# Optimization experiments

Measured on AMD Instinct MI355X. Metric: run time of the kernel, lower is better.

## Reference

```python
import jax, jax.numpy as jnp
import numpy as np

T, IN, M, C, OUT = 8192, 1024, 64, 16, 1024  # time, input, trace, context, output


def _ln(x, eps=1e-5):
    mu = jnp.mean(x, axis=-1, keepdims=True)
    var = jnp.var(x, axis=-1, keepdims=True)
    return (x - mu) * jax.lax.rsqrt(var + eps)


def _mish(x):
    return x * jnp.tanh(jax.nn.softplus(x))


def setup_inputs() -> dict:
    key = jax.random.key(0)
    ks = jax.random.split(key, 8)

    def w(k, o, i):
        return (jax.random.normal(k, (o, i), jnp.float32) / np.sqrt(i).astype(np.float32))

    return {
        "x": jax.random.normal(ks[0], (T, IN), jnp.float32),
        "state0": jnp.zeros((1, M, C), jnp.float32),  # real part of complex zero init
        "start": jax.random.uniform(ks[1], (T,)) < 0.002,  # sparse episode resets
        "next_done": jnp.zeros((T,), bool),  # unused by the sequential-equivalent math
        "a": jnp.linspace(1e-6, 0.5, M, dtype=jnp.float32),  # ffa.init decay
        "bf": (2.0 * jnp.pi / jnp.linspace(1.0, 1024.0, C)).astype(jnp.float32),  # ffa.init freqs
        "pre_w": w(ks[2], M, IN), "pre_b": jnp.zeros((M,), jnp.float32),
        "skip_w": w(ks[3], OUT, IN), "skip_b": jnp.zeros((OUT,), jnp.float32),
        "mix_w1": w(ks[4], M * C, 2 * M * C), "mix_b1": jnp.zeros((M * C,), jnp.float32),
        "mix_w2": w(ks[5], M * C, M * C), "mix_b2": jnp.zeros((M * C,), jnp.float32),
        "mix_w3": w(ks[6], OUT, M * C), "mix_b3": jnp.zeros((OUT,), jnp.float32),
    }


def _forward(x, state0, start, a, bf, pre_w, pre_b, skip_w, skip_b,
             mix_w1, mix_b1, mix_w2, mix_b2, mix_w3, mix_b3):
    Tn = x.shape[0]
    # pre = softplus(Linear(LayerNorm(x)))  -> [T, M]
    pre = jax.nn.softplus(_ln(x) @ pre_w.T + pre_b)
    # one-step FFA decay gamma[m,c] = exp(-|a_m| + i*b_c)
    la = jnp.broadcast_to(-jnp.abs(a)[:, None], (a.shape[0], bf.shape[0]))
    lb = jnp.broadcast_to(bf[None, :], la.shape)
    gamma = jnp.exp(jax.lax.complex(la, lb))  # [M, C] complex64
    # reset monoid: s_t = A_t * s_{t-1} + b_t,  A_t = 0 where episode starts
    A = jnp.where(start[:, None, None], jnp.zeros((), gamma.dtype), gamma[None])  # [T,M,C]
    b_el = jnp.broadcast_to(pre[:, :, None].astype(gamma.dtype), A.shape)  # [T,M,C]
    s_init = state0.astype(gamma.dtype)  # [1, M, C]
    b_el = b_el.at[0].add(A[0] * s_init[0])  # fold carried state into first element

    def combine(lhs, rhs):
        Al, bl = lhs
        Ar, br = rhs
        return Ar * Al, Ar * bl + br

    _, s = jax.lax.associative_scan(combine, (A, b_el))  # s: [T, M, C] states at every t

    s_flat = s.reshape(Tn, M * C)
    # global (all-element) complex mean / real std normalization, as in the source
    scaled = (s_flat - jnp.mean(s_flat)) / (1e-6 + jnp.std(s_flat))
    z = jnp.concatenate([scaled.real, scaled.imag], axis=-1)  # [T, 2*M*C]
    z = _mish(z @ mix_w1.T + mix_b1)
    z = _mish(z @ mix_w2.T + mix_b2)
    z = z @ mix_w3.T + mix_b3  # [T, OUT]
    out = _ln(z + (x @ skip_w.T + skip_b))
    return out, s[-1:]


def reference(x, state0, start, next_done, a, bf, pre_w, pre_b, skip_w, skip_b,
              mix_w1, mix_b1, mix_w2, mix_b2, mix_w3, mix_b3):
    return _forward(x, state0, start, a, bf, pre_w, pre_b, skip_w, skip_b,
                    mix_w1, mix_b1, mix_w2, mix_b2, mix_w3, mix_b3)
```

## Files before the change

### kernel.cpp

```cpp
#include <hip/hip_runtime.h>
#include <hip/hip_bf16.h>

#define T_    8192
#define INDIM 1024
#define MTR   64
#define CCTX  16
#define MC    1024
#define NOUT  1024
#define CHUNK 64
#define NCH   128

using bf16x8 = __attribute__((ext_vector_type(8))) short;
using f32x4  = __attribute__((ext_vector_type(4))) float;

__device__ __forceinline__ unsigned short f2bf(float f) {
  unsigned int u = __builtin_bit_cast(unsigned int, f);
  u += 0x7fffu + ((u >> 16) & 1u);
  return (unsigned short)(u >> 16);
}
__device__ __forceinline__ float bf2f(unsigned short u) {
  return __builtin_bit_cast(float, (unsigned int)u << 16);
}

__device__ __forceinline__ float mish_f(float v) {
  float u = __expf(v);
  float w = u * (u + 2.f);
  return (v > 20.f) ? v : v * __fdividef(w, w + 2.f);
}

typedef __attribute__((address_space(1))) void gas_void;
typedef __attribute__((address_space(3))) void las_void;

__device__ __forceinline__ void gload_lds16(const void* g, void* l) {
  __builtin_amdgcn_global_load_lds((gas_void*)g, (las_void*)l, 16, 0, 0);
}

__device__ __forceinline__ float2 block_sum2(float s, float ss, float* sbuf) {
#pragma unroll
  for (int off = 32; off > 0; off >>= 1) {
    s  += __shfl_down(s, off);
    ss += __shfl_down(ss, off);
  }
  if ((threadIdx.x & 63) == 0) {
    sbuf[(threadIdx.x >> 6) * 2]     = s;
    sbuf[(threadIdx.x >> 6) * 2 + 1] = ss;
  }
  __syncthreads();
  return make_float2(sbuf[0] + sbuf[2] + sbuf[4] + sbuf[6],
                     sbuf[1] + sbuf[3] + sbuf[5] + sbuf[7]);
}

__global__ __launch_bounds__(256) void prep_k(const float* __restrict__ w1, const float* __restrict__ w2,
                                              const float* __restrict__ w3, const float* __restrict__ sw,
                                              const float* __restrict__ x,
                                              unsigned short* __restrict__ o1, unsigned short* __restrict__ o2,
                                              unsigned short* __restrict__ o3, unsigned short* __restrict__ o4,
                                              float* __restrict__ wre, float* __restrict__ wim,
                                              float2* __restrict__ rowstat, unsigned short* __restrict__ xb) {
  __shared__ float sbuf[8];
  const int b = blockIdx.x;
  if (b < 5120) {
    long i = ((long)b * 256 + threadIdx.x) * 4;
    const float* src; unsigned short* dst; long off;
    if (i < 2097152)      { src = w1; dst = o1; off = i; }
    else if (i < 3145728) { src = w2; dst = o2; off = i - 2097152; }
    else if (i < 4194304) { src = w3; dst = o3; off = i - 3145728; }
    else if (i < 5242880) { src = sw; dst = o4; off = i - 4194304; }
    else return;
    float4 v = *(const float4*)(src + off);
    ushort4 o = { f2bf(v.x), f2bf(v.y), f2bf(v.z), f2bf(v.w) };
    *(ushort4*)(dst + off) = o;
  } else if (b < 6144) {
    const long row = b - 5120;
    const float4* r4 = (const float4*)(w1 + row * 2048);
    float4 a = r4[threadIdx.x];
    float4 c = r4[256 + threadIdx.x];
    float2 t = block_sum2(a.x + a.y + a.z + a.w, c.x + c.y + c.z + c.w, sbuf);
    if (threadIdx.x == 0) { wre[row] = t.x; wim[row] = t.y; }
  } else {
    const long row = b - 6144;
    float4 v = ((const float4*)(x + (row << 10)))[threadIdx.x];
    ushort4 c = { f2bf(v.x), f2bf(v.y), f2bf(v.z), f2bf(v.w) };
    ((ushort4*)(xb + (row << 10)))[threadIdx.x] = c;
    float2 t = block_sum2(v.x + v.y + v.z + v.w,
                          v.x * v.x + v.y * v.y + v.z * v.z + v.w * v.w, sbuf);
    float mean = t.x * (1.f / 1024.f);
    float var  = t.y * (1.f / 1024.f) - mean * mean;
    float rstd = rsqrtf(var + 1e-5f);
    if (threadIdx.x == 0) rowstat[row] = make_float2(mean, rstd);
  }
}

__global__ __launch_bounds__(256) void ln_out1b_k(const unsigned short* __restrict__ p, float* __restrict__ out) {
  __shared__ float sbuf[8];
  const long row = blockIdx.x;
  ushort4 u4 = ((const ushort4*)(p + (row << 10)))[threadIdx.x];
  float4 v = { bf2f(u4.x), bf2f(u4.y), bf2f(u4.z), bf2f(u4.w) };
  float2 t = block_sum2(v.x + v.y + v.z + v.w,
                        v.x * v.x + v.y * v.y + v.z * v.z + v.w * v.w, sbuf);
  float mean = t.x * (1.f / 1024.f);
  float var  = t.y * (1.f / 1024.f) - mean * mean;
  float rstd = rsqrtf(var + 1e-5f);
  float4 o = { (v.x - mean) * rstd, (v.y - mean) * rstd,
               (v.z - mean) * rstd, (v.w - mean) * rstd };
  ((float4*)(out + (row << 10)))[threadIdx.x] = o;
}

__global__ __launch_bounds__(256) void pre_part_k(const float* __restrict__ x,
                                                  const float2* __restrict__ rowstat,
                                                  const float* __restrict__ pw,
                                                  float* __restrict__ part) {
  const int lane = threadIdx.x & 63;
  const int wvu  = __builtin_amdgcn_readfirstlane(threadIdx.x >> 6);
  const int kc   = blockIdx.y;
  const int r0   = (blockIdx.x * 4 + wvu) * 32;

  const float* wrow = pw + (long)lane * 1024 + kc * 128;
  float wreg[128];
#pragma unroll
  for (int j = 0; j < 32; ++j)
    *(float4*)&wreg[j * 4] = ((const float4*)wrow)[j];
  float swsum = 0.f;
#pragma unroll
  for (int j = 0; j < 128; ++j) swsum += wreg[j];

  float* po = part + ((long)kc * T_ + r0) * 64 + lane;
  const float* xbase = x + (long)r0 * 1024 + kc * 128;

  for (int i = 0; i < 32; i += 2) {
    const float4* xr0 = (const float4*)(xbase + (long)i * 1024);
    const float4* xr1 = (const float4*)(xbase + (long)(i + 1) * 1024);
    float a0 = 0.f, a1 = 0.f, a2 = 0.f, a3 = 0.f;
    float b0 = 0.f, b1 = 0.f, b2 = 0.f, b3 = 0.f;
#pragma unroll
    for (int j = 0; j < 32; j += 4) {
      float4 xa0 = xr0[j],     xa1 = xr0[j + 1], xa2 = xr0[j + 2], xa3 = xr0[j + 3];
      float4 xb0 = xr1[j],     xb1 = xr1[j + 1], xb2 = xr1[j + 2], xb3 = xr1[j + 3];
      a0 += wreg[4*j+0]*xa0.x  + wreg[4*j+1]*xa0.y  + wreg[4*j+2]*xa0.z  + wreg[4*j+3]*xa0.w;
      a1 += wreg[4*j+4]*xa1.x  + wreg[4*j+5]*xa1.y  + wreg[4*j+6]*xa1.z  + wreg[4*j+7]*xa1.w;
      a2 += wreg[4*j+8]*xa2.x  + wreg[4*j+9]*xa2.y  + wreg[4*j+10]*xa2.z + wreg[4*j+11]*xa2.w;
      a3 += wreg[4*j+12]*xa3.x + wreg[4*j+13]*xa3.y + wreg[4*j+14]*xa3.z + wreg[4*j+15]*xa3.w;
      b0 += wreg[4*j+0]*xb0.x  + wreg[4*j+1]*xb0.y  + wreg[4*j+2]*xb0.z  + wreg[4*j+3]*xb0.w;
      b1 += wreg[4*j+4]*xb1.x  + wreg[4*j+5]*xb1.y  + wreg[4*j+6]*xb1.z  + wreg[4*j+7]*xb1.w;
      b2 += wreg[4*j+8]*xb2.x  + wreg[4*j+9]*xb2.y  + wreg[4*j+10]*xb2.z + wreg[4*j+11]*xb2.w;
      b3 += wreg[4*j+12]*xb3.x + wreg[4*j+13]*xb3.y + wreg[4*j+14]*xb3.z + wreg[4*j+15]*xb3.w;
    }
    float2 s0 = rowstat[r0 + i];
    float2 s1 = rowstat[r0 + i + 1];
    po[(long)i * 64]       = s0.y * ((a0 + a1) + (a2 + a3)) - s0.x * s0.y * swsum;
    po[(long)(i + 1) * 64] = s1.y * ((b0 + b1) + (b2 + b3)) - s1.x * s1.y * swsum;
  }
}

__global__ __launch_bounds__(256) void pre_fin_k(const float* __restrict__ part,
                                                 const float* __restrict__ pb,
                                                 float* __restrict__ pre) {
  long i = (long)blockIdx.x * 256 + threadIdx.x;
  int m = (int)(i & 63);
  float s = 0.f;
#pragma unroll
  for (int kc = 0; kc < 8; ++kc)
    s += part[(long)kc * T_ * 64 + i];
  float v = s + pb[m];
  float sp = fmaxf(v, 0.f) + log1pf(expf(-fabsf(v)));
  pre[i] = sp;
}

__global__ __launch_bounds__(256) void scan_p1(const float* __restrict__ pre, const int* __restrict__ start,
                                               const float* __restrict__ a, const float* __restrict__ bfr,
                                               double2* __restrict__ chA, double2* __restrict__ chB) {
  int ch = blockIdx.y * 256 + threadIdx.x;
  int m = ch >> 4, c = ch & 15;
  double dec = exp(-fabs((double)a[m]));
  double th = (double)bfr[c];
  double gre = dec * cos(th), gim = dec * sin(th);
  int j = blockIdx.x;
  int t0 = j * CHUNK;
  double pr = 1.0, pi = 0.0, sr = 0.0, si = 0.0;
  for (int t = t0; t < t0 + CHUNK; ++t) {
    double b = (double)pre[(long)t * 64 + m];
    if (start[t]) {
      pr = 0.0; pi = 0.0; sr = b; si = 0.0;
    } else {
      double nsr = gre * sr - gim * si + b;
      si = gre * si + gim * sr; sr = nsr;
      double npr = gre * pr - gim * pi;
      pi = gre * pi + gim * pr; pr = npr;
    }
  }
  chA[j * MC + ch] = make_double2(pr, pi);
  chB[j * MC + ch] = make_double2(sr, si);
}

__global__ __launch_bounds__(64) void scan_p2(const double2* __restrict__ chA, const double2* __restrict__ chB,
                                              const float* __restrict__ state0,
                                              double2* __restrict__ carry, double* __restrict__ red,
                                              float* __restrict__ out_tail, int fmt) {
  if (blockIdx.x == 0 && threadIdx.x < 4) red[threadIdx.x] = 0.0;
  int ch = blockIdx.x * 64 + threadIdx.x;
  double cr = (double)state0[ch], ci = 0.0;
  for (int j = 0; j < NCH; ++j) {
    carry[j * MC + ch] = make_double2(cr, ci);
    double2 A = chA[j * MC + ch];
    double2 B = chB[j * MC + ch];
    double ncr = A.x * cr - A.y * ci + B.x;
    ci = A.x * ci + A.y * cr + B.y;
    cr = ncr;
  }
  if (fmt == 1024) {
    out_tail[ch] = (float)cr;
  } else {
    out_tail[2 * ch]     = (float)cr;
    out_tail[2 * ch + 1] = (float)ci;
  }
}

__global__ __launch_bounds__(256) void scan_p3(const float* __restrict__ pre, const int* __restrict__ start,
                                               const float* __restrict__ a, const float* __restrict__ bfr,
                                               const double2* __restrict__ carry,
                                               double* __restrict__ red,
                                               unsigned short* __restrict__ z) {
  __shared__ double sbuf[12];
  int ch = blockIdx.y * 256 + threadIdx.x;
  int m = ch >> 4, c = ch & 15;
  double dec = exp(-fabs((double)a[m]));
  double th = (double)bfr[c];
  double gre = dec * cos(th), gim = dec * sin(th);
  int j = blockIdx.x;
  int t0 = j * CHUNK;
  double2 cin = carry[j * MC + ch];
  double sr = cin.x, si = cin.y;
  double aR = 0.0, aI = 0.0, aS = 0.0;
  for (int t = t0; t < t0 + CHUNK; ++t) {
    double b = (double)pre[(long)t * 64 + m];
    if (start[t]) { sr = b; si = 0.0; }
    else {
      double nsr = gre * sr - gim * si + b;
      si = gre * si + gim * sr; sr = nsr;
    }
    z[(long)t * 2048 + ch]        = f2bf((float)sr);
    z[(long)t * 2048 + 1024 + ch] = f2bf((float)si);
    aR += sr; aI += si; aS += sr * sr + si * si;
  }
#pragma unroll
  for (int off = 32; off > 0; off >>= 1) {
    aR += __shfl_down(aR, off); aI += __shfl_down(aI, off); aS += __shfl_down(aS, off);
  }
  if ((threadIdx.x & 63) == 0) {
    int w = threadIdx.x >> 6;
    sbuf[w * 3] = aR; sbuf[w * 3 + 1] = aI; sbuf[w * 3 + 2] = aS;
  }
  __syncthreads();
  if (threadIdx.x == 0) {
    atomicAdd(&red[0], sbuf[0] + sbuf[3] + sbuf[6] + sbuf[9]);
    atomicAdd(&red[1], sbuf[1] + sbuf[4] + sbuf[7] + sbuf[10]);
    atomicAdd(&red[2], sbuf[2] + sbuf[5] + sbuf[8] + sbuf[11]);
  }
}

__global__ void finalize_red(const double* __restrict__ red, float* __restrict__ redf) {
  const double n = (double)T_ * (double)MC;
  double mre = red[0] / n, mim = red[1] / n;
  double var = red[2] / n - mre * mre - mim * mim;
  double sd = sqrt(var > 0.0 ? var : 0.0);
  redf[0] = (float)mre;
  redf[1] = (float)mim;
  redf[2] = (float)(1.0 / (1e-6 + sd));
}

#define TSZ (128 * 32)
template<int EP>
__device__ __forceinline__ void gemm128_core(const unsigned short* __restrict__ A,
                                             const unsigned short* __restrict__ B,
                                             const float* __restrict__ bias,
                                             const unsigned short* __restrict__ addb,
                                             const float* __restrict__ redf,
                                             const float* __restrict__ wre,
                                             const float* __restrict__ wim,
                                             void* __restrict__ Cout,
                                             int bx, int by, int N_, int K_,
                                             unsigned short* lA, unsigned short* lB) {
  const int tid = threadIdx.x;
  const int lane = tid & 63;
  const int wv = tid >> 6;
  const int wr = wv >> 1, wc = wv & 1;
  const long brow = (long)bx * 128;
  const long bcol = (long)by * 128;

  f32x4 acc[4][4];
#pragma unroll
  for (int i = 0; i < 4; i++)
#pragma unroll
    for (int j = 0; j < 4; j++)
      acc[i][j] = f32x4{0.f, 0.f, 0.f, 0.f};

  const int c0 = tid, c1 = tid + 256;
  const long ar0 = brow + (c0 >> 2), ar1 = brow + (c1 >> 2);
  const long br0 = bcol + (c0 >> 2), br1 = bcol + (c1 >> 2);
  const int ko0 = (((c0 & 3) ^ ((c0 >> 3) & 3)) * 8);
  const int ko1 = (((c1 & 3) ^ ((c1 >> 3) & 3)) * 8);
  const int r15 = lane & 15;
  const int swzq = (((lane >> 4) ^ ((r15 >> 1) & 3)) * 8);

  const int nt = K_ >> 5;

#define STAGE(ti, bu)                                                      \
  do {                                                                     \
    gload_lds16(A + ar0 * K_ + (ti) * 32 + ko0, lA + (bu) * TSZ + c0 * 8); \
    gload_lds16(A + ar1 * K_ + (ti) * 32 + ko1, lA + (bu) * TSZ + c1 * 8); \
    gload_lds16(B + br0 * K_ + (ti) * 32 + ko0, lB + (bu) * TSZ + c0 * 8); \
    gload_lds16(B + br1 * K_ + (ti) * 32 + ko1, lB + (bu) * TSZ + c1 * 8); \
  } while (0)

  STAGE(0, 0);
  STAGE(1, 1);

  for (int i = 0; i < nt; ++i) {
    if (i + 2 < nt) {
      STAGE(i + 2, (i + 2) & 3);
      asm volatile("s_waitcnt vmcnt(8)" ::: "memory");
    } else if (i + 1 < nt) {
      asm volatile("s_waitcnt vmcnt(4)" ::: "memory");
    } else {
      asm volatile("s_waitcnt vmcnt(0)" ::: "memory");
    }
    __builtin_amdgcn_sched_barrier(0);
    __builtin_amdgcn_s_barrier();
    __builtin_amdgcn_sched_barrier(0);

    const unsigned short* bA = lA + (i & 3) * TSZ;
    const unsigned short* bB = lB + (i & 3) * TSZ;
    bf16x8 af[4], bv[4];
#pragma unroll
    for (int mi = 0; mi < 4; mi++)
      af[mi] = *(const bf16x8*)&bA[(wr * 64 + mi * 16 + r15) * 32 + swzq];
#pragma unroll
    for (int nj = 0; nj < 4; nj++)
      bv[nj] = *(const bf16x8*)&bB[(wc * 64 + nj * 16 + r15) * 32 + swzq];
    __builtin_amdgcn_s_setprio(1);
#pragma unroll
    for (int mi = 0; mi < 4; mi++)
#pragma unroll
      for (int nj = 0; nj < 4; nj++)
        acc[mi][nj] = __builtin_amdgcn_mfma_f32_16x16x32_bf16(af[mi], bv[nj], acc[mi][nj], 0, 0, 0);
    __builtin_amdgcn_s_setprio(0);
  }
#undef STAGE

  float cre = 0.f, cim = 0.f, inv = 1.f;
  if (EP == 4) { cre = redf[0]; cim = redf[1]; inv = redf[2]; }

  const int rq = (lane >> 4) * 4;
#pragma unroll
  for (int nj = 0; nj < 4; nj++) {
    const long col = bcol + wc * 64 + nj * 16 + r15;
    const float bs = bias[col];
    float wrc = 0.f, wic = 0.f;
    if (EP == 4) { wrc = wre[col]; wic = wim[col]; }
#pragma unroll
    for (int mi = 0; mi < 4; mi++) {
#pragma unroll
      for (int r = 0; r < 4; r++) {
        const long row = brow + wr * 64 + mi * 16 + rq + r;
        float va = acc[mi][nj][r];
        if (EP == 1) {
          ((unsigned short*)Cout)[row * N_ + col] = f2bf(va + bs);
        } else if (EP == 3) {
          float v = va + bs + bf2f(addb[row * N_ + col]);
          ((unsigned short*)Cout)[row * N_ + col] = f2bf(v);
        } else if (EP == 4) {
          float v = (va - cre * wrc - cim * wic) * inv + bs;
          ((unsigned short*)Cout)[row * N_ + col] = f2bf(mish_f(v));
        } else {
          ((unsigned short*)Cout)[row * N_ + col] = f2bf(mish_f(va + bs));
        }
      }
    }
  }
}

template<int EP>
__global__ __launch_bounds__(256) void gemm128_k(const unsigned short* __restrict__ A,
                                                 const unsigned short* __restrict__ B,
                                                 const float* __restrict__ bias,
                                                 const unsigned short* __restrict__ addb,
                                                 void* __restrict__ Cout, int N_, int K_) {
  __shared__ __align__(16) unsigned short lA[4 * TSZ];
  __shared__ __align__(16) unsigned short lB[4 * TSZ];
  gemm128_core<EP>(A, B, bias, addb, nullptr, nullptr, nullptr, Cout,
                   blockIdx.x, blockIdx.y, N_, K_, lA, lB);
}

__global__ __launch_bounds__(256) void gemm_dual128(const unsigned short* __restrict__ A1,
                                                    const unsigned short* __restrict__ B1,
                                                    const float* __restrict__ bias1,
                                                    unsigned short* __restrict__ C1, int K1,
                                                    const float* __restrict__ redf,
                                                    const float* __restrict__ wre,
                                                    const float* __restrict__ wim,
                                                    const unsigned short* __restrict__ A2,
                                                    const unsigned short* __restrict__ B2,
                                                    const float* __restrict__ bias2,
                                                    unsigned short* __restrict__ C2, int K2) {
  __shared__ __align__(16) unsigned short lA[4 * TSZ];
  __shared__ __align__(16) unsigned short lB[4 * TSZ];
  int b = blockIdx.x;
  if (b < 512) {
    gemm128_core<4>(A1, B1, bias1, nullptr, redf, wre, wim, C1, b & 63, b >> 6, 1024, K1, lA, lB);
  } else {
    b -= 512;
    gemm128_core<1>(A2, B2, bias2, nullptr, nullptr, nullptr, nullptr, C2, b & 63, b >> 6, 1024, K2, lA, lB);
  }
}

extern "C" void kernel_launch(void* const* d_in, const int* in_sizes, int n_in,
                              void* d_out, int out_size, void* d_ws, size_t ws_size,
                              hipStream_t stream) {
  (void)in_sizes; (void)n_in; (void)ws_size;
  const float* x      = (const float*)d_in[0];
  const float* state0 = (const float*)d_in[1];
  const int*   start  = (const int*)d_in[2];
  const float* a      = (const float*)d_in[4];
  const float* bfr    = (const float*)d_in[5];
  const float* pre_w  = (const float*)d_in[6];
  const float* pre_b  = (const float*)d_in[7];
  const float* skip_w = (const float*)d_in[8];
  const float* skip_b = (const float*)d_in[9];
  const float* w1     = (const float*)d_in[10];
  const float* b1     = (const float*)d_in[11];
  const float* w2     = (const float*)d_in[12];
  const float* b2     = (const float*)d_in[13];
  const float* w3     = (const float*)d_in[14];
  const float* b3     = (const float*)d_in[15];

  char* ws = (char*)d_ws;
  const size_t MB = 1u << 20;
  unsigned short* skipb = (unsigned short*)(ws + 0);
  float*          part  = (float*)(ws + 16 * MB);
  unsigned short* h3b   = (unsigned short*)(ws + 48 * MB);
  unsigned short* z     = (unsigned short*)(ws + 64 * MB);
  unsigned short* xb    = (unsigned short*)(ws + 96 * MB);
  unsigned short* h2    = (unsigned short*)(ws + 96 * MB);
  unsigned short* h1    = (unsigned short*)(ws + 112 * MB);
  unsigned short* wb1   = (unsigned short*)(ws + 128 * MB);
  unsigned short* wb2   = (unsigned short*)(ws + 132 * MB);
  unsigned short* wb3   = (unsigned short*)(ws + 134 * MB);
  unsigned short* skwb  = (unsigned short*)(ws + 136 * MB);
  float*          pre   = (float*)(ws + 138 * MB);
  double2*        chA   = (double2*)(ws + 140 * MB);
  double2*        chB   = (double2*)(ws + 142 * MB);
  double2*        carry = (double2*)(ws + 144 * MB);
  double*         red   = (double*)(ws + 146 * MB);
  float*          redf  = (float*)(ws + 146 * MB + 64);
  float2*         rowst = (float2*)(ws + 147 * MB);
  float*          wre   = (float*)(ws + 147 * MB + 65536);
  float*          wim   = (float*)(ws + 147 * MB + 65536 + 4096);

  prep_k<<<14336, 256, 0, stream>>>(w1, w2, w3, skip_w, x,
                                    wb1, wb2, wb3, skwb, wre, wim, rowst, xb);

  pre_part_k<<<dim3(64, 8), 256, 0, stream>>>(x, rowst, pre_w, part);
  pre_fin_k<<<2048, 256, 0, stream>>>(part, pre_b, pre);

  int tail_elems = out_size - T_ * NOUT;
  float* out_tail = (float*)d_out + (long)T_ * NOUT;
  scan_p1<<<dim3(NCH, 4), 256, 0, stream>>>(pre, start, a, bfr, chA, chB);
  scan_p2<<<16, 64, 0, stream>>>(chA, chB, state0, carry, red, out_tail, tail_elems);
  scan_p3<<<dim3(NCH, 4), 256, 0, stream>>>(pre, start, a, bfr, carry, red, z);
  finalize_red<<<1, 1, 0, stream>>>(red, redf);

  gemm_dual128<<<1024, 256, 0, stream>>>(z, wb1, b1, h1, 2048, redf, wre, wim,
                                         xb, skwb, skip_b, skipb, 1024);
  gemm128_k<2><<<dim3(64, 8), 256, 0, stream>>>(h1, wb2, b2, nullptr, h2, 1024, 1024);
  gemm128_k<3><<<dim3(64, 8), 256, 0, stream>>>(h2, wb3, b3, skipb, h3b, 1024, 1024);

  ln_out1b_k<<<8192, 256, 0, stream>>>(h3b, (float*)d_out);
}
```

Before: 271.6 us.

## Load GEMM A operand straight from global into registers, skipping LDS staging

The A-tile is no longer staged through shared memory with async global-to-LDS copies. Each wave now loads its own A fragments directly into registers, with a one-iteration register prefetch (aCur/aNxt), and the wait counts are adjusted to match. This halves LDS footprint and removes the A-side LDS reads. In exchange, A data is fetched twice, since both column waves read the same rows. The per-lane 16-byte global loads are less coalesced, and A latency is hidden by only one iteration.

New measurement: 343.7 us. 1.27x slower.

```diff
diff --git a/kernel.cpp b/kernel.cpp
--- a/kernel.cpp
+++ b/kernel.cpp
@@ -279,7 +279,7 @@
                                              const float* __restrict__ wim,
                                              void* __restrict__ Cout,
                                              int bx, int by, int N_, int K_,
-                                             unsigned short* lA, unsigned short* lB) {
+                                             unsigned short* lB) {
   const int tid = threadIdx.x;
   const int lane = tid & 63;
   const int wv = tid >> 6;
@@ -295,45 +295,46 @@
       acc[i][j] = f32x4{0.f, 0.f, 0.f, 0.f};
 
   const int c0 = tid, c1 = tid + 256;
-  const long ar0 = brow + (c0 >> 2), ar1 = brow + (c1 >> 2);
   const long br0 = bcol + (c0 >> 2), br1 = bcol + (c1 >> 2);
   const int ko0 = (((c0 & 3) ^ ((c0 >> 3) & 3)) * 8);
   const int ko1 = (((c1 & 3) ^ ((c1 >> 3) & 3)) * 8);
   const int r15 = lane & 15;
+  const int kq = (lane >> 4) * 8;
   const int swzq = (((lane >> 4) ^ ((r15 >> 1) & 3)) * 8);
 
+  const unsigned short* Abase = A + (brow + wr * 64 + r15) * (long)K_ + kq;
+
   const int nt = K_ >> 5;
 
-#define STAGE(ti, bu)                                                      \
+#define STAGE_B(ti, bu)                                                    \
   do {                                                                     \
-    gload_lds16(A + ar0 * K_ + (ti) * 32 + ko0, lA + (bu) * TSZ + c0 * 8); \
-    gload_lds16(A + ar1 * K_ + (ti) * 32 + ko1, lA + (bu) * TSZ + c1 * 8); \
     gload_lds16(B + br0 * K_ + (ti) * 32 + ko0, lB + (bu) * TSZ + c0 * 8); \
     gload_lds16(B + br1 * K_ + (ti) * 32 + ko1, lB + (bu) * TSZ + c1 * 8); \
   } while (0)
 
-  STAGE(0, 0);
-  STAGE(1, 1);
+  bf16x8 aCur[4], aNxt[4];
+  STAGE_B(0, 0);
+  STAGE_B(1, 1);
+#pragma unroll
+  for (int mi = 0; mi < 4; mi++)
+    aCur[mi] = *(const bf16x8*)(Abase + (long)mi * 16 * K_);
 
   for (int i = 0; i < nt; ++i) {
-    if (i + 2 < nt) {
-      STAGE(i + 2, (i + 2) & 3);
-      asm volatile("s_waitcnt vmcnt(8)" ::: "memory");
-    } else if (i + 1 < nt) {
-      asm volatile("s_waitcnt vmcnt(4)" ::: "memory");
-    } else {
-      asm volatile("s_waitcnt vmcnt(0)" ::: "memory");
+    if (i + 2 < nt) STAGE_B(i + 2, (i + 2) & 3);
+    if (i + 1 < nt) {
+#pragma unroll
+      for (int mi = 0; mi < 4; mi++)
+        aNxt[mi] = *(const bf16x8*)(Abase + (long)mi * 16 * K_ + (i + 1) * 32);
     }
+    if (i + 2 < nt)      asm volatile("s_waitcnt vmcnt(6)" ::: "memory");
+    else if (i + 1 < nt) asm volatile("s_waitcnt vmcnt(4)" ::: "memory");
+    else                 asm volatile("s_waitcnt vmcnt(0)" ::: "memory");
     __builtin_amdgcn_sched_barrier(0);
     __builtin_amdgcn_s_barrier();
     __builtin_amdgcn_sched_barrier(0);
 
-    const unsigned short* bA = lA + (i & 3) * TSZ;
     const unsigned short* bB = lB + (i & 3) * TSZ;
-    bf16x8 af[4], bv[4];
-#pragma unroll
-    for (int mi = 0; mi < 4; mi++)
-      af[mi] = *(const bf16x8*)&bA[(wr * 64 + mi * 16 + r15) * 32 + swzq];
+    bf16x8 bv[4];
 #pragma unroll
     for (int nj = 0; nj < 4; nj++)
       bv[nj] = *(const bf16x8*)&bB[(wc * 64 + nj * 16 + r15) * 32 + swzq];
@@ -342,10 +343,13 @@
     for (int mi = 0; mi < 4; mi++)
 #pragma unroll
       for (int nj = 0; nj < 4; nj++)
-        acc[mi][nj] = __builtin_amdgcn_mfma_f32_16x16x32_bf16(af[mi], bv[nj], acc[mi][nj], 0, 0, 0);
+        acc[mi][nj] = __builtin_amdgcn_mfma_f32_16x16x32_bf16(aCur[mi], bv[nj], acc[mi][nj], 0, 0, 0);
     __builtin_amdgcn_s_setprio(0);
-  }
-#undef STAGE
+#pragma unroll
+    for (int mi = 0; mi < 4; mi++)
+      aCur[mi] = aNxt[mi];
+  }
+#undef STAGE_B
 
   float cre = 0.f, cim = 0.f, inv = 1.f;
   if (EP == 4) { cre = redf[0]; cim = redf[1]; inv = redf[2]; }
@@ -385,10 +389,9 @@
                                                  const float* __restrict__ bias,
                                                  const unsigned short* __restrict__ addb,
                                                  void* __restrict__ Cout, int N_, int K_) {
-  __shared__ __align__(16) unsigned short lA[4 * TSZ];
   __shared__ __align__(16) unsigned short lB[4 * TSZ];
   gemm128_core<EP>(A, B, bias, addb, nullptr, nullptr, nullptr, Cout,
-                   blockIdx.x, blockIdx.y, N_, K_, lA, lB);
+                   blockIdx.x, blockIdx.y, N_, K_, lB);
 }
 
 __global__ __launch_bounds__(256) void gemm_dual128(const unsigned short* __restrict__ A1,
@@ -402,14 +405,13 @@
                                                     const unsigned short* __restrict__ B2,
                                                     const float* __restrict__ bias2,
                                                     unsigned short* __restrict__ C2, int K2) {
-  __shared__ __align__(16) unsigned short lA[4 * TSZ];
   __shared__ __align__(16) unsigned short lB[4 * TSZ];
   int b = blockIdx.x;
   if (b < 512) {
-    gemm128_core<4>(A1, B1, bias1, nullptr, redf, wre, wim, C1, b & 63, b >> 6, 1024, K1, lA, lB);
+    gemm128_core<4>(A1, B1, bias1, nullptr, redf, wre, wim, C1, b & 63, b >> 6, 1024, K1, lB);
   } else {
     b -= 512;
-    gemm128_core<1>(A2, B2, bias2, nullptr, nullptr, nullptr, nullptr, C2, b & 63, b >> 6, 1024, K2, lA, lB);
+    gemm128_core<1>(A2, B2, bias2, nullptr, nullptr, nullptr, nullptr, C2, b & 63, b >> 6, 1024, K2, lB);
   }
 }
 
```
